# Optimization experiments

Measured on AMD Instinct MI355X. Metric: run time of the kernel, lower is better.

The kernel has to match this reference:

```python
import jax, jax.numpy as jnp
import numpy as np

B, N, D = 4, 2048, 512
OUT, H = 512, 8
HD = OUT // H

def setup_inputs() -> dict:
    key = jax.random.key(0)
    ks = jax.random.split(key, 10)
    s = 1.0 / np.sqrt(D)
    x = jax.random.normal(ks[0], (B, N, D), dtype=jnp.float32)
    adj = jax.random.randint(ks[1], (N, N), 0, 2, dtype=jnp.int32)
    Wq = jax.random.uniform(ks[2], (D, OUT), jnp.float32, -s, s)
    bq = jax.random.uniform(ks[3], (OUT,), jnp.float32, -s, s)
    Wk = jax.random.uniform(ks[4], (D, OUT), jnp.float32, -s, s)
    bk = jax.random.uniform(ks[5], (OUT,), jnp.float32, -s, s)
    Wv = jax.random.uniform(ks[6], (D, OUT), jnp.float32, -s, s)
    bv = jax.random.uniform(ks[7], (OUT,), jnp.float32, -s, s)
    so = 1.0 / np.sqrt(OUT)
    Wo = jax.random.uniform(ks[8], (OUT, OUT), jnp.float32, -so, so)
    bo = jax.random.uniform(ks[9], (OUT,), jnp.float32, -so, so)
    return {"x": x, "adj": adj, "Wq": Wq, "bq": bq, "Wk": Wk, "bk": bk,
            "Wv": Wv, "bv": bv, "Wo": Wo, "bo": bo}

def reference(x, adj, Wq, bq, Wk, bk, Wv, bv, Wo, bo):
    scale = HD ** -0.5
    # [B,N,OUT] -> [B,H,N,HD]
    def split_heads(t):
        return t.reshape(B, N, H, HD).transpose(0, 2, 1, 3)
    q = split_heads(x @ Wq + bq)
    k = split_heads(x @ Wk + bk)
    v = split_heads(x @ Wv + bv)
    attn = jnp.einsum('bhnd,bhmd->bhnm', q, k) * scale  # [B,H,N,N]
    mask = (adj == 0)[None, None, :, :]
    attn = jnp.where(mask, jnp.float32(-1e9), attn)
    attn = jax.nn.softmax(attn, axis=-1)
    out = jnp.einsum('bhnm,bhmd->bhnd', attn, v)
    out = out.transpose(0, 2, 1, 3).reshape(B, N, OUT)
    return out @ Wo + bo
```

## Files before the change

### kernel.cpp

```cpp
#include <hip/hip_runtime.h>
#include <math.h>

#define NB   4
#define NN   2048
#define DD   512
#define NOUT 512
#define NH   8
#define HDIM 64

typedef __attribute__((ext_vector_type(4))) short bf16x4;
typedef __attribute__((ext_vector_type(8))) short bf16x8;
typedef __attribute__((ext_vector_type(4))) float f32x4;
#define MFMA32(a, b, c)  __builtin_amdgcn_mfma_f32_16x16x32_bf16(a, b, c, 0, 0, 0)

typedef const __attribute__((address_space(1))) unsigned int* gas_ptr;
typedef __attribute__((address_space(3))) unsigned int* las_ptr;

#define SCALE2 0.18033688f


__device__ inline unsigned short f2bf(float f) {
    unsigned int u = __float_as_uint(f);
    u += 0x7fffu + ((u >> 16) & 1u);
    return (unsigned short)(u >> 16);
}

__device__ inline unsigned int pack_trunc(float lo, float hi) {
    return __builtin_amdgcn_perm(__float_as_uint(hi), __float_as_uint(lo), 0x07060302u);
}

#if __has_builtin(__builtin_amdgcn_exp2f)
#define EXP2(x) __builtin_amdgcn_exp2f(x)
#else
#define EXP2(x) exp2f(x)
#endif

__global__ __launch_bounds__(256) void prep(
    const float* __restrict__ x, unsigned short* __restrict__ xt,
    const float* __restrict__ W0, const float* __restrict__ W1,
    const float* __restrict__ W2, const float* __restrict__ W3,
    unsigned short* __restrict__ Tqkv, unsigned short* __restrict__ To,
    const int* __restrict__ adj, unsigned int* __restrict__ amaskW)
{
    const int blk = blockIdx.x;
    const int t   = threadIdx.x;

    if (blk < 2048) {
        const int i = (blk * 256 + t) * 8;
        const int m = i >> 9, k = i & 511;
        float4 a = *(const float4*)(x + i);
        float4 b = *(const float4*)(x + i + 4);
        ushort4 u0, u1;
        u0.x = f2bf(a.x); u0.y = f2bf(a.y); u0.z = f2bf(a.z); u0.w = f2bf(a.w);
        u1.x = f2bf(b.x); u1.y = f2bf(b.y); u1.z = f2bf(b.z); u1.w = f2bf(b.w);
        unsigned short* dst = xt + ((size_t)(m >> 7) * 65536)
                                 + (k >> 5) * 4096 + (m & 127) * 32 + (k & 31);
        *(ushort4*)dst       = u0;
        *(ushort4*)(dst + 4) = u1;
        return;
    }
    if (blk < 2304) {
        __shared__ float tile[64][65];
        const int idx = blk - 2048;
        const int z = idx >> 6, rem = idx & 63;
        const float* W;
        switch (z) {
            case 0:  W = W0; break;
            case 1:  W = W1; break;
            case 2:  W = W2; break;
            default: W = W3; break;
        }
        unsigned short* T = (z < 3) ? Tqkv : To;
        const int ngbase  = (z < 3) ? z * 512 : 0;
        const int k0 = (rem & 7) * 64, n0 = (rem >> 3) * 64;
        const int r = t >> 6, c = t & 63;
#pragma unroll
        for (int rep = 0; rep < 16; ++rep) {
            const int row = rep * 4 + r;
            tile[row][c] = W[(size_t)(k0 + row) * NOUT + n0 + c];
        }
        __syncthreads();
        const int k  = k0 + c;
        const int ks = k >> 5, kk = k & 31;
#pragma unroll
        for (int rep = 0; rep < 16; ++rep) {
            const int row = rep * 4 + r;
            const int ng  = ngbase + n0 + row;
            T[((size_t)(ng >> 7) * 65536) + ks * 4096 + (ng & 127) * 32 + kk]
                = f2bf(tile[c][row]);
        }
        return;
    }
    {
        const int gid  = (blk - 2304) * 256 + t;
        const int w0   = gid * 4;
        const int qrow = w0 >> 10;
        const int wloc = w0 & 1023;
        const int kb0  = wloc * 2;
        int4 a0 = *(const int4*)(adj + (size_t)qrow * NN + kb0);
        int4 a1 = *(const int4*)(adj + (size_t)qrow * NN + kb0 + 4);
        uint4 m;
        m.x = (a0.x ? 0xFFFFu : 0u) | (a0.y ? 0xFFFF0000u : 0u);
        m.y = (a0.z ? 0xFFFFu : 0u) | (a0.w ? 0xFFFF0000u : 0u);
        m.z = (a1.x ? 0xFFFFu : 0u) | (a1.y ? 0xFFFF0000u : 0u);
        m.w = (a1.z ? 0xFFFFu : 0u) | (a1.w ? 0xFFFF0000u : 0u);
        *(uint4*)(amaskW + (size_t)qrow * 1024 + wloc) = m;
    }
}

#define GT_SETUP(Atil, Wtil)                                                   \
    const int t = threadIdx.x, wave = t >> 6, lane = t & 63;                   \
    const int quad = lane >> 4, l16 = lane & 15;                               \
    const int _orig = blockIdx.y * gridDim.x + blockIdx.x;                     \
    const int _nwg  = gridDim.x * gridDim.y;                                   \
    const int _swz  = (_orig & 7) * (_nwg >> 3) + (_orig >> 3);                \
    const int bx = _swz % gridDim.x, by = _swz / gridDim.x;                    \
    const int n0 = bx * 128, m0 = by * 128;                                    \
    const int wm = (wave & 1) * 64, wn = (wave >> 1) * 64;                     \
    const unsigned short* aP[4];                                               \
    const unsigned short* bP[4];                                               \
    _Pragma("unroll")                                                          \
    for (int mt = 0; mt < 4; ++mt)                                             \
        aP[mt] = Atil + (size_t)by * 65536                                     \
               + (wm + mt * 16 + l16) * 32 + quad * 8;                         \
    _Pragma("unroll")                                                          \
    for (int nt = 0; nt < 4; ++nt)                                             \
        bP[nt] = Wtil + (size_t)bx * 65536                                     \
               + (wn + nt * 16 + l16) * 32 + quad * 8;

#define GT_LOADF(Af, Bf, NTC, ks)                                              \
    _Pragma("unroll")                                                          \
    for (int mt = 0; mt < 4; ++mt) Af[mt] = *(const bf16x8*)(aP[mt] + (ks) * 4096); \
    _Pragma("unroll")                                                          \
    for (int nt = 0; nt < NTC; ++nt) Bf[nt] = *(const bf16x8*)(bP[nt] + (ks) * 4096);

#define GT_MFMA(Af, Bf, NTC)                                                   \
    _Pragma("unroll")                                                          \
    for (int mt = 0; mt < 4; ++mt)                                             \
        _Pragma("unroll")                                                      \
        for (int nt = 0; nt < NTC; ++nt)                                       \
            acc[mt][nt] = MFMA32(Af[mt], Bf[nt], acc[mt][nt]);

#define GT_LOOP(NTC)                                                           \
    f32x4 acc[4][NTC];                                                         \
    _Pragma("unroll")                                                          \
    for (int mt = 0; mt < 4; ++mt)                                             \
        _Pragma("unroll")                                                      \
        for (int nt = 0; nt < NTC; ++nt) acc[mt][nt] = (f32x4){0.f, 0.f, 0.f, 0.f}; \
    bf16x8 aA[4], bA[NTC], aB[4], bB[NTC];                                     \
    GT_LOADF(aA, bA, NTC, 0);                                                  \
    for (int kk = 0; kk < 8; ++kk) {                                           \
        GT_LOADF(aB, bB, NTC, 2 * kk + 1);                                     \
        GT_MFMA(aA, bA, NTC);                                                  \
        if (kk < 7) { GT_LOADF(aA, bA, NTC, 2 * kk + 2); }                     \
        GT_MFMA(aB, bB, NTC);                                                  \
    }

__global__ __launch_bounds__(256, 3) void gemm_qkv(
    const unsigned short* __restrict__ Atil,
    const unsigned short* __restrict__ Wtil,
    const float* __restrict__ bq, const float* __restrict__ bk,
    const float* __restrict__ bv,
    unsigned short* __restrict__ qo, unsigned short* __restrict__ ko,
    unsigned short* __restrict__ vto)
{
    __shared__ unsigned short eps[4 * 2560];
    GT_SETUP(Atil, Wtil);
    GT_LOOP(4);

    const int seg   = n0 >> 9;
    const int nloc0 = n0 & 511;
    const float* bp = (seg == 0) ? bq : (seg == 1) ? bk : bv;
    unsigned short* dst3 = (seg == 0) ? qo : (seg == 1) ? ko : vto;
    const int h = (nloc0 + wn) >> 6;

    float bias4[4];
#pragma unroll
    for (int nt = 0; nt < 4; ++nt) bias4[nt] = bp[nloc0 + wn + nt * 16 + l16];

    unsigned short* Lo = eps + wave * 2560;
#pragma unroll
    for (int mt = 0; mt < 4; ++mt) {
        if (seg < 2) {
#pragma unroll
            for (int nt = 0; nt < 4; ++nt)
#pragma unroll
                for (int r = 0; r < 4; ++r) {
                    float val = acc[mt][nt][r] + bias4[nt];
                    if (seg == 0) val *= SCALE2;
                    Lo[(quad * 4 + r) * 72 + nt * 16 + l16] = f2bf(val);
                }
#pragma unroll
            for (int pass = 0; pass < 2; ++pass) {
                const int row = pass * 8 + (lane >> 3);
                const int mg  = m0 + wm + mt * 16 + row;
                const int bb  = mg >> 11, n = mg & (NN - 1);
                bf16x8 v = *(const bf16x8*)&Lo[row * 72 + (lane & 7) * 8];
                *(bf16x8*)(dst3 + ((size_t)(bb * NH + h) * NN + n) * HDIM
                           + (lane & 7) * 8) = v;
            }
        } else {
#pragma unroll
            for (int nt = 0; nt < 4; ++nt)
#pragma unroll
                for (int r = 0; r < 4; ++r) {
                    const float val = acc[mt][nt][r] + bias4[nt];
                    Lo[(nt * 16 + l16) * 40 + quad * 4 + r] = f2bf(val);
                }
            const int d  = lane;
            const int mg = m0 + wm + mt * 16;
            const int bb = mg >> 11, n = mg & (NN - 1);
            unsigned short* dr = dst3 + ((size_t)(bb * NH + h) * HDIM + d) * NN + n;
            *(bf16x8*)dr       = *(const bf16x8*)&Lo[d * 40];
            *(bf16x8*)(dr + 8) = *(const bf16x8*)&Lo[d * 40 + 8];
        }
    }
}

__global__ __launch_bounds__(256, 3) void gemm_o(
    const unsigned short* __restrict__ Atil,
    const unsigned short* __restrict__ Wtil,
    const float* __restrict__ bias,
    float* __restrict__ C)
{
    const int t = threadIdx.x, wave = t >> 6, lane = t & 63;
    const int quad = lane >> 4, l16 = lane & 15;
    const int _orig = blockIdx.y * gridDim.x + blockIdx.x;
    const int _nwg  = gridDim.x * gridDim.y;
    const int _swz  = (_orig & 7) * (_nwg >> 3) + (_orig >> 3);
    const int bx = _swz % gridDim.x, by = _swz / gridDim.x;
    const int n0 = bx * 64, m0 = by * 128;
    const int wm = (wave & 1) * 64, wn = (wave >> 1) * 32;
    const unsigned short* aP[4];
    const unsigned short* bP[2];
#pragma unroll
    for (int mt = 0; mt < 4; ++mt)
        aP[mt] = Atil + (size_t)by * 65536
               + (wm + mt * 16 + l16) * 32 + quad * 8;
#pragma unroll
    for (int nt = 0; nt < 2; ++nt)
        bP[nt] = Wtil + (size_t)(n0 >> 7) * 65536
               + ((n0 & 64) + wn + nt * 16 + l16) * 32 + quad * 8;

    GT_LOOP(2);

    float bias2[2];
#pragma unroll
    for (int nt = 0; nt < 2; ++nt) bias2[nt] = bias[n0 + wn + nt * 16 + l16];

#pragma unroll
    for (int mt = 0; mt < 4; ++mt)
#pragma unroll
        for (int nt = 0; nt < 2; ++nt) {
            const int col = n0 + wn + nt * 16 + l16;
#pragma unroll
            for (int r = 0; r < 4; ++r) {
                const int row = m0 + wm + mt * 16 + quad * 4 + r;
                C[(size_t)row * NOUT + col] = acc[mt][nt][r] + bias2[nt];
            }
        }
}

__global__ __launch_bounds__(512, 4) void attn_mfma(
    const unsigned short* __restrict__ qg,
    const unsigned short* __restrict__ kg,
    const unsigned short* __restrict__ vt,
    const unsigned int* __restrict__ amask,
    unsigned short* __restrict__ aot)
{
    __shared__ unsigned short smem[18432];
    unsigned short* Ka = smem;
    unsigned short* Va = smem + 4096;
    unsigned short* Kb = smem + 8192;
    unsigned short* Vb = smem + 12288;

    const int t    = threadIdx.x;
    const int wave = t >> 6;
    const int lane = t & 63;
    const int quad = lane >> 4;
    const int l16  = lane & 15;
    const int pair = wave >> 1;
    const int hk   = wave & 1;

    const int qt = blockIdx.x, h = blockIdx.y, b = blockIdx.z;
    const int bh = b * NH + h;
    const int q0 = qt * 128;

    const unsigned short* kbase  = kg + (size_t)bh * NN * HDIM;
    const unsigned short* vtbase = vt + (size_t)bh * HDIM * NN;

    const int drow = lane >> 3;
    const int dblk = (lane & 7) ^ drow;
    const int p  = wave * 8 + drow;
    const int Lp = (p & 32) + ((p >> 2) & 3) * 8 + ((p >> 4) & 1) * 4 + (p & 3);

    const int sw  = l16 & 7;
    const int bo0 = (quad ^ sw) * 8;
    const int bo1 = bo0 ^ 32;

#define ATT_ISSUE(kt, Kd, Vd)                                                  \
    {                                                                          \
        const int r0 = wave * 8;                                               \
        __builtin_amdgcn_global_load_lds(                                      \
            (gas_ptr)(kbase + (size_t)((kt) * 64 + Lp) * HDIM + dblk * 8),     \
            (las_ptr)(Kd + r0 * 64), 16, 0, 0);                                \
        __builtin_amdgcn_global_load_lds(                                      \
            (gas_ptr)(vtbase + (size_t)(r0 + drow) * NN + (kt) * 64 + dblk * 8), \
            (las_ptr)(Vd + r0 * 64), 16, 0, 0);                                \
    }

    const int myq0 = q0 + pair * 32 + l16;
    const int myq1 = myq0 + 16;
    const unsigned short* qrow0 = qg + ((size_t)bh * NN + myq0) * HDIM;
    const unsigned short* qrow1 = qg + ((size_t)bh * NN + myq1) * HDIM;
    const bf16x8 bQ0g0 = *(const bf16x8*)(qrow0 + quad * 8);
    const bf16x8 bQ1g0 = *(const bf16x8*)(qrow0 + quad * 8 + 32);
    const bf16x8 bQ0g1 = *(const bf16x8*)(qrow1 + quad * 8);
    const bf16x8 bQ1g1 = *(const bf16x8*)(qrow1 + quad * 8 + 32);

    const unsigned int* mrow0 = amask + (size_t)myq0 * 1024 + quad * 4;
    const unsigned int* mrow1 = amask + (size_t)myq1 * 1024 + quad * 4;
#define MLOAD(kt, g) (*(const uint4*)(((g) ? mrow1 : mrow0) + (kt) * 32 + hk * 16))

    bf16x8 ones8;
#pragma unroll
    for (int j = 0; j < 8; ++j) ones8[j] = (short)0x3F80;

    f32x4 O[4][2];
#pragma unroll
    for (int dt = 0; dt < 4; ++dt)
#pragma unroll
        for (int g = 0; g < 2; ++g) O[dt][g] = (f32x4){0.f, 0.f, 0.f, 0.f};
    f32x4 lacc[2];
    lacc[0] = (f32x4){0.f, 0.f, 0.f, 0.f};
    lacc[1] = (f32x4){0.f, 0.f, 0.f, 0.f};

    auto tile = [&](const unsigned short* Ks, const unsigned short* Vs,
                    uint4 mwg0, uint4 mwg1) {
        bf16x8 aK[2][2];
#pragma unroll
        for (int kg = 0; kg < 2; ++kg) {
            const int nt = hk * 2 + kg;
            aK[kg][0] = *(const bf16x8*)&Ks[(nt * 16 + l16) * 64 + bo0];
            aK[kg][1] = *(const bf16x8*)&Ks[(nt * 16 + l16) * 64 + bo1];
        }
        bf16x8 Pt[2];
#pragma unroll
        for (int g = 0; g < 2; ++g) {
            const uint4 mw = g ? mwg1 : mwg0;
            const bf16x8 q0f = g ? bQ0g1 : bQ0g0;
            const bf16x8 q1f = g ? bQ1g1 : bQ1g0;
            union { unsigned int u[4]; bf16x8 v; } cv;
#pragma unroll
            for (int kg = 0; kg < 2; ++kg) {
                f32x4 s = (f32x4){0.f, 0.f, 0.f, 0.f};
                s = MFMA32(aK[kg][0], q0f, s);
                s = MFMA32(aK[kg][1], q1f, s);
                const float p0 = EXP2(s[0]);
                const float p1 = EXP2(s[1]);
                const float p2 = EXP2(s[2]);
                const float p3 = EXP2(s[3]);
                cv.u[kg * 2 + 0] = pack_trunc(p0, p1) & (kg ? mw.z : mw.x);
                cv.u[kg * 2 + 1] = pack_trunc(p2, p3) & (kg ? mw.w : mw.y);
            }
            Pt[g] = cv.v;
            lacc[g] = MFMA32(ones8, Pt[g], lacc[g]);
        }
#pragma unroll
        for (int dt = 0; dt < 4; ++dt) {
            bf16x8 aV = *(const bf16x8*)
                &Vs[(dt * 16 + l16) * 64 + (((hk * 4 + quad) ^ sw) * 8)];
#pragma unroll
            for (int g = 0; g < 2; ++g)
                O[dt][g] = MFMA32(aV, Pt[g], O[dt][g]);
        }
    };

    uint4 mA0 = MLOAD(0, 0), mA1 = MLOAD(0, 1);
    uint4 mB0, mB1;
    ATT_ISSUE(0, Ka, Va);
    for (int kk = 0; kk < 16; ++kk) {
        __syncthreads();
        ATT_ISSUE(2 * kk + 1, Kb, Vb);
        mB0 = MLOAD(2 * kk + 1, 0); mB1 = MLOAD(2 * kk + 1, 1);
        tile(Ka, Va, mA0, mA1);
        __syncthreads();
        if (kk < 15) {
            ATT_ISSUE(2 * kk + 2, Ka, Va);
            mA0 = MLOAD(2 * kk + 2, 0); mA1 = MLOAD(2 * kk + 2, 1);
        }
        tile(Kb, Vb, mB0, mB1);
    }
    __syncthreads();

    float* F   = (float*)smem;
    float* myF = F + ((size_t)pair * 64 + lane) * 36;
    if (hk == 1) {
#pragma unroll
        for (int dt = 0; dt < 4; ++dt)
#pragma unroll
            for (int g = 0; g < 2; ++g)
                *(f32x4*)(myF + dt * 8 + g * 4) = O[dt][g];
        myF[32] = lacc[0][0];
        myF[33] = lacc[1][0];
    }
    __syncthreads();
    float inv0 = 0.f, inv1 = 0.f;
    if (hk == 0) {
#pragma unroll
        for (int dt = 0; dt < 4; ++dt)
#pragma unroll
            for (int g = 0; g < 2; ++g) {
                const f32x4 o2 = *(const f32x4*)(myF + dt * 8 + g * 4);
                O[dt][g] += o2;
            }
        inv0 = 1.f / (lacc[0][0] + myF[32]);
        inv1 = 1.f / (lacc[1][0] + myF[33]);
    }
    __syncthreads();

    if (hk == 0) {
#pragma unroll
        for (int g = 0; g < 2; ++g) {
            const float inv = g ? inv1 : inv0;
            unsigned short* Lo = smem + (pair * 2 + g) * 1152;
#pragma unroll
            for (int dt = 0; dt < 4; ++dt) {
                const float v0 = O[dt][g][0] * inv, v1 = O[dt][g][1] * inv;
                const float v2 = O[dt][g][2] * inv, v3 = O[dt][g][3] * inv;
                *(unsigned int*)&Lo[l16 * 72 + dt * 16 + quad * 4]     = pack_trunc(v0, v1);
                *(unsigned int*)&Lo[l16 * 72 + dt * 16 + quad * 4 + 2] = pack_trunc(v2, v3);
            }
            const int rr = lane >> 2;
            const int qq = q0 + pair * 32 + g * 16 + rr;
            const int m  = b * NN + qq;
            const int mb = m >> 7, r = m & 127;
#pragma unroll
            for (int i = 0; i < 2; ++i) {
                const int ch = (lane & 3) + 4 * i;
                const int ks = h * 2 + (ch >> 2);
                bf16x8 val = *(const bf16x8*)&Lo[rr * 72 + ch * 8];
                *(bf16x8*)(aot + (size_t)mb * 65536 + ks * 4096 + r * 32 + (ch & 3) * 8) = val;
            }
        }
    }
#undef ATT_ISSUE
#undef MLOAD
}

extern "C" void kernel_launch(void* const* d_in, const int* in_sizes, int n_in,
                              void* d_out, int out_size, void* d_ws, size_t ws_size,
                              hipStream_t stream)
{
    const float* x   = (const float*)d_in[0];
    const int*   adj = (const int*)  d_in[1];
    const float* Wq  = (const float*)d_in[2];
    const float* bq  = (const float*)d_in[3];
    const float* Wk  = (const float*)d_in[4];
    const float* bk  = (const float*)d_in[5];
    const float* Wv  = (const float*)d_in[6];
    const float* bv  = (const float*)d_in[7];
    const float* Wo  = (const float*)d_in[8];
    const float* bo  = (const float*)d_in[9];
    float* out = (float*)d_out;

    const size_t qkv_elems = (size_t)NB * NH * NN * HDIM;
    unsigned short* xt    = (unsigned short*)d_ws;
    unsigned short* q     = xt   + qkv_elems;
    unsigned short* kb    = q    + qkv_elems;
    unsigned short* vtb   = kb   + qkv_elems;
    unsigned short* tWqkv = vtb  + qkv_elems;
    unsigned short* tWo   = tWqkv + (size_t)3 * DD * NOUT;
    unsigned int*   amaskW = (unsigned int*)(tWo + (size_t)DD * NOUT);
    unsigned short* aot   = xt;

    prep<<<dim3(4352), 256, 0, stream>>>(x, xt, Wq, Wk, Wv, Wo,
                                         tWqkv, tWo, adj, amaskW);

    gemm_qkv<<<dim3(12, 64), 256, 0, stream>>>(xt, tWqkv, bq, bk, bv, q, kb, vtb);

    attn_mfma<<<dim3(NN / 128, NH, NB), 512, 0, stream>>>(q, kb, vtb, amaskW, aot);

    gemm_o<<<dim3(8, 64), 256, 0, stream>>>(aot, tWo, bo, out);
}
```

Before: 190.7 us.

## Stage GEMM tiles through LDS with async global_load_lds double buffering

The QKV and output projection GEMMs now copy A and B tiles into double-buffered shared memory with direct global-to-LDS loads and an XOR swizzle, then read MFMA fragments from LDS. Previously each wave loaded its fragments straight from global memory, so data shared across waves was fetched redundantly. The workgroup-order swizzle for L2 locality is removed, and the change adds two block barriers per k-step plus LDS bank-conflict exposure.

```diff
diff --git a/kernel.cpp b/kernel.cpp
--- a/kernel.cpp
+++ b/kernel.cpp
@@ -34,6 +34,8 @@
 #else
 #define EXP2(x) exp2f(x)
 #endif
+
+#define SWZB(g) ((g) ^ (((g) >> 3) & 7))
 
 __global__ __launch_bounds__(256) void prep(
     const float* __restrict__ x, unsigned short* __restrict__ xt,
@@ -108,31 +110,24 @@
     }
 }
 
-#define GT_SETUP(Atil, Wtil)                                                   \
-    const int t = threadIdx.x, wave = t >> 6, lane = t & 63;                   \
-    const int quad = lane >> 4, l16 = lane & 15;                               \
-    const int _orig = blockIdx.y * gridDim.x + blockIdx.x;                     \
-    const int _nwg  = gridDim.x * gridDim.y;                                   \
-    const int _swz  = (_orig & 7) * (_nwg >> 3) + (_orig >> 3);                \
-    const int bx = _swz % gridDim.x, by = _swz / gridDim.x;                    \
-    const int n0 = bx * 128, m0 = by * 128;                                    \
-    const int wm = (wave & 1) * 64, wn = (wave >> 1) * 64;                     \
-    const unsigned short* aP[4];                                               \
-    const unsigned short* bP[4];                                               \
-    _Pragma("unroll")                                                          \
-    for (int mt = 0; mt < 4; ++mt)                                             \
-        aP[mt] = Atil + (size_t)by * 65536                                     \
-               + (wm + mt * 16 + l16) * 32 + quad * 8;                         \
-    _Pragma("unroll")                                                          \
-    for (int nt = 0; nt < 4; ++nt)                                             \
-        bP[nt] = Wtil + (size_t)bx * 65536                                     \
-               + (wn + nt * 16 + l16) * 32 + quad * 8;
-
-#define GT_LOADF(Af, Bf, NTC, ks)                                              \
-    _Pragma("unroll")                                                          \
-    for (int mt = 0; mt < 4; ++mt) Af[mt] = *(const bf16x8*)(aP[mt] + (ks) * 4096); \
-    _Pragma("unroll")                                                          \
-    for (int nt = 0; nt < NTC; ++nt) Bf[nt] = *(const bf16x8*)(bP[nt] + (ks) * 4096);
+#define GTS_STAGE(ks, Ab, Bb, NB16)                                            \
+    {                                                                          \
+        const unsigned short* As_ = Asrc + (ks) * 4096;                        \
+        const unsigned short* Bs_ = Bsrc + (ks) * 4096;                        \
+        __builtin_amdgcn_global_load_lds(                                      \
+            (gas_ptr)(As_ + (wave * 64 + lswz) * 8),                           \
+            (las_ptr)((Ab) + wave * 512), 16, 0, 0);                           \
+        __builtin_amdgcn_global_load_lds(                                      \
+            (gas_ptr)(As_ + (256 + wave * 64 + lswz) * 8),                     \
+            (las_ptr)((Ab) + 2048 + wave * 512), 16, 0, 0);                    \
+        __builtin_amdgcn_global_load_lds(                                      \
+            (gas_ptr)(Bs_ + (wave * 64 + lswz) * 8),                           \
+            (las_ptr)((Bb) + wave * 512), 16, 0, 0);                           \
+        if ((NB16) == 512)                                                     \
+            __builtin_amdgcn_global_load_lds(                                  \
+                (gas_ptr)(Bs_ + (256 + wave * 64 + lswz) * 8),                 \
+                (las_ptr)((Bb) + 2048 + wave * 512), 16, 0, 0);                \
+    }
 
 #define GT_MFMA(Af, Bf, NTC)                                                   \
     _Pragma("unroll")                                                          \
@@ -141,19 +136,35 @@
         for (int nt = 0; nt < NTC; ++nt)                                       \
             acc[mt][nt] = MFMA32(Af[mt], Bf[nt], acc[mt][nt]);
 
-#define GT_LOOP(NTC)                                                           \
+#define GTS_FRAGS(Ab, Bb, NTC)                                                 \
+    bf16x8 aF[4], bF[NTC];                                                     \
+    _Pragma("unroll")                                                          \
+    for (int mt = 0; mt < 4; ++mt) aF[mt] = *(const bf16x8*)&(Ab)[aOff[mt]];   \
+    _Pragma("unroll")                                                          \
+    for (int nt = 0; nt < NTC; ++nt) bF[nt] = *(const bf16x8*)&(Bb)[bOff[nt]];
+
+#define GTS_LOOP(NTC, NB16, sA0, sB0, sA1, sB1)                                \
+    const int lswz = lane ^ ((lane >> 3) & 7);                                 \
+    int aOff[4], bOff[NTC];                                                    \
+    _Pragma("unroll")                                                          \
+    for (int mt = 0; mt < 4; ++mt)                                             \
+        aOff[mt] = SWZB((wm + mt * 16 + l16) * 4 + quad) * 8;                  \
+    _Pragma("unroll")                                                          \
+    for (int nt = 0; nt < NTC; ++nt)                                           \
+        bOff[nt] = SWZB((wn + nt * 16 + l16) * 4 + quad) * 8;                  \
     f32x4 acc[4][NTC];                                                         \
     _Pragma("unroll")                                                          \
     for (int mt = 0; mt < 4; ++mt)                                             \
         _Pragma("unroll")                                                      \
         for (int nt = 0; nt < NTC; ++nt) acc[mt][nt] = (f32x4){0.f, 0.f, 0.f, 0.f}; \
-    bf16x8 aA[4], bA[NTC], aB[4], bB[NTC];                                     \
-    GT_LOADF(aA, bA, NTC, 0);                                                  \
+    GTS_STAGE(0, sA0, sB0, NB16);                                              \
     for (int kk = 0; kk < 8; ++kk) {                                           \
-        GT_LOADF(aB, bB, NTC, 2 * kk + 1);                                     \
-        GT_MFMA(aA, bA, NTC);                                                  \
-        if (kk < 7) { GT_LOADF(aA, bA, NTC, 2 * kk + 2); }                     \
-        GT_MFMA(aB, bB, NTC);                                                  \
+        __syncthreads();                                                       \
+        GTS_STAGE(2 * kk + 1, sA1, sB1, NB16);                                 \
+        { GTS_FRAGS(sA0, sB0, NTC); GT_MFMA(aF, bF, NTC); }                    \
+        __syncthreads();                                                       \
+        if (kk < 7) GTS_STAGE(2 * kk + 2, sA0, sB0, NB16);                     \
+        { GTS_FRAGS(sA1, sB1, NTC); GT_MFMA(aF, bF, NTC); }                    \
     }
 
 __global__ __launch_bounds__(256, 3) void gemm_qkv(
@@ -164,9 +175,20 @@
     unsigned short* __restrict__ qo, unsigned short* __restrict__ ko,
     unsigned short* __restrict__ vto)
 {
-    __shared__ unsigned short eps[4 * 2560];
-    GT_SETUP(Atil, Wtil);
-    GT_LOOP(4);
+    __shared__ unsigned short smem[16384];
+    unsigned short* sA0 = smem;
+    unsigned short* sB0 = smem + 4096;
+    unsigned short* sA1 = smem + 8192;
+    unsigned short* sB1 = smem + 12288;
+
+    const int t = threadIdx.x, wave = t >> 6, lane = t & 63;
+    const int quad = lane >> 4, l16 = lane & 15;
+    const int n0 = blockIdx.x * 128, m0 = blockIdx.y * 128;
+    const int wm = (wave & 1) * 64, wn = (wave >> 1) * 64;
+    const unsigned short* Asrc = Atil + (size_t)blockIdx.y * 65536;
+    const unsigned short* Bsrc = Wtil + (size_t)blockIdx.x * 65536;
+
+    GTS_LOOP(4, 512, sA0, sB0, sA1, sB1);
 
     const int seg   = n0 >> 9;
     const int nloc0 = n0 & 511;
@@ -178,7 +200,8 @@
 #pragma unroll
     for (int nt = 0; nt < 4; ++nt) bias4[nt] = bp[nloc0 + wn + nt * 16 + l16];
 
-    unsigned short* Lo = eps + wave * 2560;
+    __syncthreads();
+    unsigned short* Lo = smem + wave * 2560;
 #pragma unroll
     for (int mt = 0; mt < 4; ++mt) {
         if (seg < 2) {
@@ -223,26 +246,20 @@
     const float* __restrict__ bias,
     float* __restrict__ C)
 {
+    __shared__ unsigned short smem[12288];
+    unsigned short* sA0 = smem;
+    unsigned short* sB0 = smem + 4096;
+    unsigned short* sA1 = smem + 6144;
+    unsigned short* sB1 = smem + 10240;
+
     const int t = threadIdx.x, wave = t >> 6, lane = t & 63;
     const int quad = lane >> 4, l16 = lane & 15;
-    const int _orig = blockIdx.y * gridDim.x + blockIdx.x;
-    const int _nwg  = gridDim.x * gridDim.y;
-    const int _swz  = (_orig & 7) * (_nwg >> 3) + (_orig >> 3);
-    const int bx = _swz % gridDim.x, by = _swz / gridDim.x;
-    const int n0 = bx * 64, m0 = by * 128;
+    const int n0 = blockIdx.x * 64, m0 = blockIdx.y * 128;
     const int wm = (wave & 1) * 64, wn = (wave >> 1) * 32;
-    const unsigned short* aP[4];
-    const unsigned short* bP[2];
-#pragma unroll
-    for (int mt = 0; mt < 4; ++mt)
-        aP[mt] = Atil + (size_t)by * 65536
-               + (wm + mt * 16 + l16) * 32 + quad * 8;
-#pragma unroll
-    for (int nt = 0; nt < 2; ++nt)
-        bP[nt] = Wtil + (size_t)(n0 >> 7) * 65536
-               + ((n0 & 64) + wn + nt * 16 + l16) * 32 + quad * 8;
-
-    GT_LOOP(2);
+    const unsigned short* Asrc = Atil + (size_t)blockIdx.y * 65536;
+    const unsigned short* Bsrc = Wtil + (size_t)(n0 >> 7) * 65536 + (n0 & 64) * 32;
+
+    GTS_LOOP(2, 256, sA0, sB0, sA1, sB1);
 
     float bias2[2];
 #pragma unroll
```

After: 174.0 us, median of 3. 1.1x faster.
